# Kernel optimization log

Measured on AMD Instinct MI355X. Metric: run time of the kernel, lower is better.

## Reference

```python
import jax, jax.numpy as jnp
import numpy as np

N_SLOTS, SLOT_DIM, FEAT_DIM, N_HEADS = 8, 256, 128, 4
HEAD_DIM = SLOT_DIM // N_HEADS
B, H, W = 32, 64, 64


def layernorm(x, g, b, eps=1e-5):
    mu = jnp.mean(x, axis=-1, keepdims=True)
    var = jnp.var(x, axis=-1, keepdims=True)
    return (x - mu) * jax.lax.rsqrt(var + eps) * g + b


def setup_inputs() -> dict:
    key = jax.random.key(0)
    ks = jax.random.split(key, 20)
    s = lambda i, shape, sc: (jax.random.normal(ks[i], shape, dtype=jnp.float32) * sc)
    return {
        'features': s(0, (B, FEAT_DIM, H, W), 1.0),
        'slots': s(1, (B, N_SLOTS, SLOT_DIM), 1.0),
        'Wq': s(2, (SLOT_DIM, SLOT_DIM), 0.05), 'bq': jnp.zeros((SLOT_DIM,), jnp.float32),
        'Wk': s(3, (FEAT_DIM, SLOT_DIM), 0.05), 'bk': jnp.zeros((SLOT_DIM,), jnp.float32),
        'Wv': s(4, (FEAT_DIM, SLOT_DIM), 0.05), 'bv': jnp.zeros((SLOT_DIM,), jnp.float32),
        'W_ih': s(5, (3 * SLOT_DIM, SLOT_DIM), 0.05), 'b_ih': jnp.zeros((3 * SLOT_DIM,), jnp.float32),
        'W_hh': s(6, (3 * SLOT_DIM, SLOT_DIM), 0.05), 'b_hh': jnp.zeros((3 * SLOT_DIM,), jnp.float32),
        'g_pre': jnp.ones((SLOT_DIM,), jnp.float32), 'b_pre': jnp.zeros((SLOT_DIM,), jnp.float32),
        'g_post': jnp.ones((SLOT_DIM,), jnp.float32), 'b_post': jnp.zeros((SLOT_DIM,), jnp.float32),
        'W1': s(7, (SLOT_DIM, 2 * SLOT_DIM), 0.05), 'b1': jnp.zeros((2 * SLOT_DIM,), jnp.float32),
        'W2': s(8, (2 * SLOT_DIM, SLOT_DIM), 0.05), 'b2': jnp.zeros((SLOT_DIM,), jnp.float32),
    }


def reference(features, slots, Wq, bq, Wk, bk, Wv, bv, W_ih, b_ih, W_hh, b_hh,
              g_pre, b_pre, g_post, b_post, W1, b1, W2, b2):
    b, c, h, w = features.shape
    n = h * w
    feats = features.transpose(0, 2, 3, 1).reshape(b, n, c)  # (B, HW, C)

    slots_n = layernorm(slots, g_pre, b_pre)
    q = (slots_n @ Wq + bq).reshape(b, N_SLOTS, N_HEADS, HEAD_DIM)
    k = (feats @ Wk + bk).reshape(b, n, N_HEADS, HEAD_DIM)
    v = (feats @ Wv + bv).reshape(b, n, N_HEADS, HEAD_DIM)

    scale = HEAD_DIM ** -0.5
    # scores: (B, heads, slots, HW); softmax over the SLOT axis (competition)
    scores = jnp.einsum('bshd,bnhd->bhsn', q, k) * scale
    attn = jax.nn.softmax(scores, axis=2)
    agg = jnp.einsum('bhsn,bnhd->bshd', attn, v).reshape(b, N_SLOTS, SLOT_DIM)

    # GRUCell (torch semantics): gates ordered r, z, n
    x = agg.reshape(b * N_SLOTS, SLOT_DIM)
    hprev = slots.reshape(b * N_SLOTS, SLOT_DIM)
    gi = x @ W_ih.T + b_ih
    gh = hprev @ W_hh.T + b_hh
    i_r, i_z, i_n = jnp.split(gi, 3, axis=-1)
    h_r, h_z, h_n = jnp.split(gh, 3, axis=-1)
    r = jax.nn.sigmoid(i_r + h_r)
    z = jax.nn.sigmoid(i_z + h_z)
    nn_ = jnp.tanh(i_n + r * h_n)
    hnew = (1.0 - z) * nn_ + z * hprev
    updated = hnew.reshape(b, N_SLOTS, SLOT_DIM)

    # post-norm + MLP residual (dropout is identity in eval)
    refined = jax.nn.relu(layernorm(updated, g_post, b_post) @ W1 + b1) @ W2 + b2
    return updated + refined
```

## Files before the change

kernel.cpp:

```cpp
#include <hip/hip_runtime.h>
#include <hip/hip_bf16.h>

#define NSLOT 8
#define SDIM 256
#define FDIM 128
#define NHEAD 4
#define HDIM 64
#define NPOS 4096

typedef short v8s __attribute__((ext_vector_type(8)));
typedef short v4s __attribute__((ext_vector_type(4)));
typedef float v4f __attribute__((ext_vector_type(4)));

__device__ __forceinline__ unsigned short f2bf(float x) {
    __hip_bfloat16 h = __float2bfloat16(x);
    unsigned short u; __builtin_memcpy(&u, &h, 2); return u;
}
__device__ __forceinline__ float bfr2f(unsigned short u) {
    __hip_bfloat16 h; __builtin_memcpy(&h, &u, 2); return __bfloat162float(h);
}
__device__ __forceinline__ void splitf(float x, unsigned short& hi, unsigned short& lo) {
    hi = f2bf(x);
    lo = f2bf(x - bfr2f(hi));
}

__global__ __launch_bounds__(256) void k_prep(
    const float* __restrict__ slots,
    const float* __restrict__ Wq, const float* __restrict__ bq,
    const float* __restrict__ g_pre, const float* __restrict__ b_pre,
    const float* __restrict__ Wk, const float* __restrict__ bk,
    const float* __restrict__ W1, const float* __restrict__ W2,
    const float* __restrict__ W_ih, const float* __restrict__ W_hh,
    const float* __restrict__ Wv,
    unsigned short* __restrict__ qkT_ws, float* __restrict__ qb_ws,
    unsigned short* __restrict__ W1Th, unsigned short* __restrict__ W1Tl,
    unsigned short* __restrict__ W2Th, unsigned short* __restrict__ W2Tl,
    unsigned short* __restrict__ WihH, unsigned short* __restrict__ WihL,
    unsigned short* __restrict__ WhhH, unsigned short* __restrict__ WhhL,
    unsigned short* __restrict__ WvTH, unsigned short* __restrict__ WvTl,
    float* __restrict__ agg_ws)
{
    int blk = blockIdx.x, t = threadIdx.x;
    __shared__ float s_ln[8 * 256];
    __shared__ float q_l[32 * 65];
    __shared__ float red1[256], red2[256];
    __shared__ float tl[32][33];

    if (blk >= 560) {
        int id3 = blk - 560;
        int k0 = (id3 & 3) * 32, n0 = (id3 >> 2) * 32;
        for (int i = 0; i < 4; i++) {
            int idx = i * 256 + t, r = idx >> 5, c = idx & 31;
            tl[r][c] = Wv[(size_t)(k0 + r) * 256 + n0 + c];
        }
        __syncthreads();
        for (int i = 0; i < 4; i++) {
            int idx = i * 256 + t, r = idx >> 5, c = idx & 31;
            unsigned short hi, lo; splitf(tl[c][r], hi, lo);
            WvTH[(size_t)(n0 + r) * 128 + k0 + c] = hi;
            WvTl[(size_t)(n0 + r) * 128 + k0 + c] = lo;
        }
        return;
    }
    if (blk >= 512) {
        int id2 = blk - 512;
        const float* src; unsigned short *dh, *dl; int r0;
        if (id2 < 24) { src = W_ih; dh = WihH; dl = WihL; r0 = id2 * 32; }
        else          { src = W_hh; dh = WhhH; dl = WhhL; r0 = (id2 - 24) * 32; }
        for (int i = 0; i < 32; i++) {
            size_t idx = (size_t)(r0 + i) * 256 + t;
            unsigned short hi, lo; splitf(src[idx], hi, lo);
            dh[idx] = hi; dl[idx] = lo;
        }
        return;
    }
    if (blk >= 256) {
        int id = blk - 256;
        const float* src; unsigned short *dh, *dl; int N, K, k0, n0;
        if (id < 128) { src = W1; dh = W1Th; dl = W1Tl; N = 512; K = 256;
                        k0 = (id >> 4) * 32; n0 = (id & 15) * 32; }
        else          { int i2 = id - 128; src = W2; dh = W2Th; dl = W2Tl; N = 256; K = 512;
                        k0 = (i2 >> 3) * 32; n0 = (i2 & 7) * 32; }
        for (int i = 0; i < 4; i++) {
            int idx = i * 256 + t, r = idx >> 5, c = idx & 31;
            tl[r][c] = src[(size_t)(k0 + r) * N + n0 + c];
        }
        __syncthreads();
        for (int i = 0; i < 4; i++) {
            int idx = i * 256 + t, r = idx >> 5, c = idx & 31;
            unsigned short hi, lo; splitf(tl[c][r], hi, lo);
            dh[(size_t)(n0 + r) * K + k0 + c] = hi;
            dl[(size_t)(n0 + r) * K + k0 + c] = lo;
        }
        return;
    }

    int b = blk >> 3, chunk = blk & 7;
    if (chunk == 0)
        for (int i = 0; i < 8; i++) agg_ws[b * 2048 + i * 256 + t] = 0.0f;

    int s8 = t >> 5, lane = t & 31;
    float xv[8], sum = 0.0f, sq = 0.0f;
    for (int u = 0; u < 8; u++) {
        float x = slots[(b * 8 + s8) * 256 + lane * 8 + u];
        xv[u] = x; sum += x; sq += x * x;
    }
    red1[t] = sum; red2[t] = sq;
    __syncthreads();
    for (int o = 16; o > 0; o >>= 1) {
        if (lane < o) { red1[t] += red1[t + o]; red2[t] += red2[t + o]; }
        __syncthreads();
    }
    float mu  = red1[s8 * 32] * (1.0f / 256);
    float var = red2[s8 * 32] * (1.0f / 256) - mu * mu;
    float rstd = rsqrtf(var + 1e-5f);
    for (int u = 0; u < 8; u++) {
        int j = lane * 8 + u;
        s_ln[s8 * 256 + j] = (xv[u] - mu) * rstd * g_pre[j] + b_pre[j];
    }
    __syncthreads();

    float qa[8];
    #pragma unroll
    for (int s = 0; s < 8; s++) qa[s] = bq[t];
    for (int k = 0; k < 256; k++) {
        float wq = Wq[k * 256 + t];
        #pragma unroll
        for (int s = 0; s < 8; s++) qa[s] += s_ln[s * 256 + k] * wq;
    }
    int h = t >> 6, d = t & 63;
    for (int s = 0; s < 8; s++) q_l[(s * 4 + h) * 65 + d] = qa[s];
    __syncthreads();

    int hs = t & 31, hh = hs >> 3, si = hs & 7, c0 = t >> 5;
    const float* qrow = &q_l[(si * 4 + hh) * 65];
    for (int i = 0; i < 2; i++) {
        int c = chunk * 16 + i * 8 + c0;
        const float4* wk4 = (const float4*)&Wk[c * 256 + hh * 64];
        float acc = 0.0f;
        #pragma unroll
        for (int d4 = 0; d4 < 16; d4++) {
            float4 w = wk4[d4];
            acc += w.x * qrow[d4 * 4] + w.y * qrow[d4 * 4 + 1]
                 + w.z * qrow[d4 * 4 + 2] + w.w * qrow[d4 * 4 + 3];
        }
        qkT_ws[(b * 32 + hs) * 128 + c] = f2bf(acc);
    }
    if (chunk == 0 && t < 32) {
        int h2 = t >> 3, s2 = t & 7;
        float acc = 0.0f;
        for (int d2 = 0; d2 < 64; d2++)
            acc += bk[h2 * 64 + d2] * q_l[(s2 * 4 + h2) * 65 + d2];
        qb_ws[b * 32 + t] = acc;
    }
}

__global__ __launch_bounds__(256, 4) void k_attn(
    const float* __restrict__ feat,
    const unsigned short* __restrict__ WvTH, const unsigned short* __restrict__ WvTl,
    const float* __restrict__ bv,
    const unsigned short* __restrict__ qkT, const float* __restrict__ qb_ws,
    float* __restrict__ agg_ws)
{
    __shared__ __align__(16) char smem[31360];
    unsigned short* featPC = (unsigned short*)smem;
    unsigned short* featCP = (unsigned short*)(smem + 8704);
    unsigned short* attFH  = (unsigned short*)smem;
    unsigned short* attFL  = (unsigned short*)(smem + 8704);
    float*          s_attn = (float*)(smem + 23040);
    unsigned short* s_aT   = (unsigned short*)(smem + 27648);
    float*          s_S    = (float*)(smem + 31232);

    int t = threadIdx.x, b = blockIdx.y, n0 = blockIdx.x * 128;
    int wv_ = t >> 6, lane = t & 63, quad = lane >> 4, l16 = lane & 15;
    int mt = wv_ >> 1, nt = wv_ & 1;
    int sp  = l16 + mt * 16;
    int shs = l16 + nt * 16;

    v8s bq_[4];
    #pragma unroll
    for (int ch = 0; ch < 4; ch++)
        bq_[ch] = *(const v8s*)&qkT[(b * 32 + shs) * 128 + ch * 32 + quad * 8];
    float qbv = qb_ws[b * 32 + shs];
    if (t < 32) s_S[t] = 0.0f;

    v4f accF[4];
    #pragma unroll
    for (int i = 0; i < 4; i++) accF[i] = (v4f){0.f, 0.f, 0.f, 0.f};

    int c0 = (t >> 3) * 4, p0 = (t & 7) * 4;

    for (int tt = 0; tt < 4; ++tt) {
        __syncthreads();
        int nb = n0 + tt * 32;
        float fv[4][4];
        #pragma unroll
        for (int r = 0; r < 4; r++) {
            float4 f = *(const float4*)&feat[(size_t)b * (FDIM * NPOS)
                                             + (size_t)(c0 + r) * NPOS + nb + p0];
            fv[r][0] = f.x; fv[r][1] = f.y; fv[r][2] = f.z; fv[r][3] = f.w;
        }
        #pragma unroll
        for (int r = 0; r < 4; r++)
            *(v4s*)&featCP[(c0 + r) * 56 + p0] =
                (v4s){(short)f2bf(fv[r][0]), (short)f2bf(fv[r][1]),
                      (short)f2bf(fv[r][2]), (short)f2bf(fv[r][3])};
        #pragma unroll
        for (int j = 0; j < 4; j++)
            *(v4s*)&featPC[(p0 + j) * 136 + c0] =
                (v4s){(short)f2bf(fv[0][j]), (short)f2bf(fv[1][j]),
                      (short)f2bf(fv[2][j]), (short)f2bf(fv[3][j])};
        __syncthreads();

        v4f acc = (v4f){0.f, 0.f, 0.f, 0.f};
        #pragma unroll
        for (int ch = 0; ch < 4; ch++) {
            v8s a = *(const v8s*)&featPC[sp * 136 + ch * 32 + quad * 8];
            acc = __builtin_amdgcn_mfma_f32_16x16x32_bf16(a, bq_[ch], acc, 0, 0, 0);
        }
        int pb = mt * 16 + quad * 4;
        #pragma unroll
        for (int r = 0; r < 4; r++)
            s_attn[(pb + r) * 36 + shs] = (acc[r] + qbv) * 0.125f;
        __syncthreads();

        if (t < 128) {
            int p = t >> 2, h2 = t & 3;
            float* a = &s_attn[p * 36 + h2 * 8];
            float m = a[0];
            for (int s = 1; s < 8; s++) m = fmaxf(m, a[s]);
            float e[8], ssum = 0.0f;
            for (int s = 0; s < 8; s++) { e[s] = __expf(a[s] - m); ssum += e[s]; }
            float inv = 1.0f / ssum;
            for (int s = 0; s < 8; s++)
                s_aT[(h2 * 8 + s) * 56 + p] = f2bf(e[s] * inv);
        }
        __syncthreads();

        v8s aA0 = *(const v8s*)&s_aT[l16 * 56 + quad * 8];
        v8s aA1 = *(const v8s*)&s_aT[(l16 + 16) * 56 + quad * 8];
        v8s bF0 = *(const v8s*)&featCP[(l16 + wv_ * 32) * 56 + quad * 8];
        v8s bF1 = *(const v8s*)&featCP[(l16 + wv_ * 32 + 16) * 56 + quad * 8];
        accF[0] = __builtin_amdgcn_mfma_f32_16x16x32_bf16(aA0, bF0, accF[0], 0, 0, 0);
        accF[1] = __builtin_amdgcn_mfma_f32_16x16x32_bf16(aA0, bF1, accF[1], 0, 0, 0);
        accF[2] = __builtin_amdgcn_mfma_f32_16x16x32_bf16(aA1, bF0, accF[2], 0, 0, 0);
        accF[3] = __builtin_amdgcn_mfma_f32_16x16x32_bf16(aA1, bF1, accF[3], 0, 0, 0);
        if (t < 32) {
            float ss = 0.0f;
            for (int p = 0; p < 32; p++) ss += bfr2f(s_aT[t * 56 + p]);
            s_S[t] += ss;
        }
    }
    __syncthreads();
    #pragma unroll
    for (int mt2 = 0; mt2 < 2; mt2++)
        #pragma unroll
        for (int ntl = 0; ntl < 2; ntl++) {
            v4f f = accF[mt2 * 2 + ntl];
            int cc = wv_ * 32 + ntl * 16 + l16;
            #pragma unroll
            for (int r = 0; r < 4; r++) {
                unsigned short hi, lo; splitf(f[r], hi, lo);
                attFH[(mt2 * 16 + quad * 4 + r) * 136 + cc] = hi;
                attFL[(mt2 * 16 + quad * 4 + r) * 136 + cc] = lo;
            }
        }
    __syncthreads();

    int h = wv_;
    int am = h * 8 + (l16 & 7);
    for (int nt2 = 0; nt2 < 4; nt2++) {
        int n = h * 64 + nt2 * 16 + l16;
        v4f acc = (v4f){0.f, 0.f, 0.f, 0.f};
        #pragma unroll
        for (int kk = 0; kk < 4; kk++) {
            int ko = kk * 32 + quad * 8;
            v8s ah = *(const v8s*)&attFH[am * 136 + ko];
            v8s al = *(const v8s*)&attFL[am * 136 + ko];
            v8s bh = *(const v8s*)&WvTH[(size_t)n * 128 + ko];
            v8s bl = *(const v8s*)&WvTl[(size_t)n * 128 + ko];
            acc = __builtin_amdgcn_mfma_f32_16x16x32_bf16(al, bh, acc, 0, 0, 0);
            acc = __builtin_amdgcn_mfma_f32_16x16x32_bf16(ah, bl, acc, 0, 0, 0);
            acc = __builtin_amdgcn_mfma_f32_16x16x32_bf16(ah, bh, acc, 0, 0, 0);
        }
        float bvn = bv[n];
        if (quad < 2) {
            #pragma unroll
            for (int r = 0; r < 4; r++) {
                int s = quad * 4 + r;
                atomicAdd(&agg_ws[b * 2048 + s * 256 + n],
                          acc[r] + s_S[h * 8 + s] * bvn);
            }
        }
    }
}

__global__ __launch_bounds__(256) void k_gate(
    const float* __restrict__ agg, const float* __restrict__ slots,
    const unsigned short* __restrict__ WihH, const unsigned short* __restrict__ WihL,
    const float* __restrict__ b_ih,
    const unsigned short* __restrict__ WhhH, const unsigned short* __restrict__ WhhL,
    const float* __restrict__ b_hh,
    float* __restrict__ G)
{
    int ntile = blockIdx.x, mtile = blockIdx.y, t = threadIdx.x;
    bool hhalf = ntile >= 12;
    int jbase = (hhalf ? ntile - 12 : ntile) * 64;
    const float* X = hhalf ? slots : agg;
    const unsigned short* BH = hhalf ? WhhH : WihH;
    const unsigned short* BL = hhalf ? WhhL : WihL;
    const float* bias = hhalf ? b_hh : b_ih;
    int gofs = hhalf ? 768 : 0;
    int m0 = mtile * 64;

    __shared__ __align__(16) unsigned short aH[64][264];
    __shared__ __align__(16) unsigned short aL[64][264];
    for (int i = 0; i < 16; i++) {
        int idx = i * 256 + t;
        int r = idx >> 6, q = idx & 63;
        float4 f = *(const float4*)&X[(size_t)(m0 + r) * 256 + q * 4];
        unsigned short h0,l0,h1,l1,h2,l2,h3,l3;
        splitf(f.x, h0, l0); splitf(f.y, h1, l1);
        splitf(f.z, h2, l2); splitf(f.w, h3, l3);
        *(v4s*)&aH[r][q * 4] = (v4s){(short)h0,(short)h1,(short)h2,(short)h3};
        *(v4s*)&aL[r][q * 4] = (v4s){(short)l0,(short)l1,(short)l2,(short)l3};
    }
    __syncthreads();

    int w = t >> 6, lane = t & 63, quad = lane >> 4, l16 = lane & 15;
    int am = w * 16 + l16;
    for (int s = 0; s < 4; s++) {
        int jrow = jbase + s * 16 + l16;
        v4f acc = (v4f){0.f, 0.f, 0.f, 0.f};
        #pragma unroll
        for (int kk = 0; kk < 8; kk++) {
            int ko = kk * 32 + quad * 8;
            v8s ah = *(const v8s*)&aH[am][ko];
            v8s al = *(const v8s*)&aL[am][ko];
            v8s bh = *(const v8s*)&BH[(size_t)jrow * 256 + ko];
            v8s bl = *(const v8s*)&BL[(size_t)jrow * 256 + ko];
            acc = __builtin_amdgcn_mfma_f32_16x16x32_bf16(al, bh, acc, 0, 0, 0);
            acc = __builtin_amdgcn_mfma_f32_16x16x32_bf16(ah, bl, acc, 0, 0, 0);
            acc = __builtin_amdgcn_mfma_f32_16x16x32_bf16(ah, bh, acc, 0, 0, 0);
        }
        float bv_ = bias[jrow];
        int gj = gofs + jbase + s * 16 + l16;
        #pragma unroll
        for (int r = 0; r < 4; r++)
            G[(size_t)(m0 + w * 16 + quad * 4 + r) * 1536 + gj] = acc[r] + bv_;
    }
}

__device__ __forceinline__ float gru1(float ir, float iz, float in_,
                                      float hr, float hz, float hn, float hp) {
    float r = 1.0f / (1.0f + __expf(-(ir + hr)));
    float z = 1.0f / (1.0f + __expf(-(iz + hz)));
    float n = tanhf(in_ + r * hn);
    return (1.0f - z) * n + z * hp;
}

__global__ __launch_bounds__(1024) void k_tail2(
    const float* __restrict__ slots, const float* __restrict__ G,
    const float* __restrict__ g_post, const float* __restrict__ b_post,
    const unsigned short* __restrict__ W1Th, const unsigned short* __restrict__ W1Tl,
    const float* __restrict__ b1,
    const unsigned short* __restrict__ W2Th, const unsigned short* __restrict__ W2Tl,
    const float* __restrict__ b2,
    float* __restrict__ hnF, float* __restrict__ out)
{
    __shared__ __align__(16) char smem[50176];
    unsigned short* lnH   = (unsigned short*)smem;
    unsigned short* lnLo  = (unsigned short*)(smem + 8448);
    unsigned short* y1H   = (unsigned short*)(smem + 16896);
    unsigned short* y1Lo  = (unsigned short*)(smem + 33536);

    int t = threadIdx.x, m0 = blockIdx.x * 16;
    int w = t >> 6, lane = t & 63, quad = lane >> 4, l16 = lane & 15;

    {
        int row = m0 + w, c0 = lane * 4;
        const float* gp = &G[(size_t)row * 1536 + c0];
        float4 gir = *(const float4*)(gp);
        float4 giz = *(const float4*)(gp + 256);
        float4 gin = *(const float4*)(gp + 512);
        float4 ghr = *(const float4*)(gp + 768);
        float4 ghz = *(const float4*)(gp + 1024);
        float4 ghn = *(const float4*)(gp + 1280);
        float4 hp  = *(const float4*)&slots[(size_t)row * 256 + c0];
        float h0 = gru1(gir.x, giz.x, gin.x, ghr.x, ghz.x, ghn.x, hp.x);
        float h1 = gru1(gir.y, giz.y, gin.y, ghr.y, ghz.y, ghn.y, hp.y);
        float h2 = gru1(gir.z, giz.z, gin.z, ghr.z, ghz.z, ghn.z, hp.z);
        float h3 = gru1(gir.w, giz.w, gin.w, ghr.w, ghz.w, ghn.w, hp.w);
        float ssum = h0 + h1 + h2 + h3;
        float ssq  = h0*h0 + h1*h1 + h2*h2 + h3*h3;
        #pragma unroll
        for (int m = 1; m <= 32; m <<= 1) {
            ssum += __shfl_xor(ssum, m, 64);
            ssq  += __shfl_xor(ssq, m, 64);
        }
        float mu = ssum * (1.0f / 256);
        float var = ssq * (1.0f / 256) - mu * mu;
        float rstd = rsqrtf(var + 1e-5f);
        float4 gp4 = *(const float4*)&g_post[c0];
        float4 bp4 = *(const float4*)&b_post[c0];
        float l0 = (h0 - mu) * rstd * gp4.x + bp4.x;
        float l1 = (h1 - mu) * rstd * gp4.y + bp4.y;
        float l2 = (h2 - mu) * rstd * gp4.z + bp4.z;
        float l3 = (h3 - mu) * rstd * gp4.w + bp4.w;
        unsigned short a0,c0s,a1,c1s,a2,c2s,a3,c3s;
        splitf(l0, a0, c0s); splitf(l1, a1, c1s);
        splitf(l2, a2, c2s); splitf(l3, a3, c3s);
        *(v4s*)&lnH[w * 264 + c0]  = (v4s){(short)a0,(short)a1,(short)a2,(short)a3};
        *(v4s*)&lnLo[w * 264 + c0] = (v4s){(short)c0s,(short)c1s,(short)c2s,(short)c3s};
        float4 hv4; hv4.x = h0; hv4.y = h1; hv4.z = h2; hv4.w = h3;
        *(float4*)&hnF[(size_t)row * 256 + c0] = hv4;
    }
    __syncthreads();

    #pragma unroll
    for (int i = 0; i < 2; i++) {
        int ntile = w * 2 + i;
        int n = ntile * 16 + l16;
        v4f acc = (v4f){0.f, 0.f, 0.f, 0.f};
        #pragma unroll
        for (int kk = 0; kk < 8; kk++) {
            int ko = kk * 32 + quad * 8;
            v8s ah = *(const v8s*)&lnH[l16 * 264 + ko];
            v8s al = *(const v8s*)&lnLo[l16 * 264 + ko];
            v8s bh = *(const v8s*)&W1Th[(size_t)n * 256 + ko];
            v8s bl = *(const v8s*)&W1Tl[(size_t)n * 256 + ko];
            acc = __builtin_amdgcn_mfma_f32_16x16x32_bf16(al, bh, acc, 0, 0, 0);
            acc = __builtin_amdgcn_mfma_f32_16x16x32_bf16(ah, bl, acc, 0, 0, 0);
            acc = __builtin_amdgcn_mfma_f32_16x16x32_bf16(ah, bh, acc, 0, 0, 0);
        }
        float bb = b1[n];
        #pragma unroll
        for (int r = 0; r < 4; r++) {
            float y = fmaxf(acc[r] + bb, 0.0f);
            unsigned short hi, lo; splitf(y, hi, lo);
            y1H[(quad * 4 + r) * 520 + n]  = hi;
            y1Lo[(quad * 4 + r) * 520 + n] = lo;
        }
    }
    __syncthreads();

    {
        int n = w * 16 + l16;
        v4f acc = (v4f){0.f, 0.f, 0.f, 0.f};
        #pragma unroll
        for (int kk = 0; kk < 16; kk++) {
            int ko = kk * 32 + quad * 8;
            v8s ah = *(const v8s*)&y1H[l16 * 520 + ko];
            v8s al = *(const v8s*)&y1Lo[l16 * 520 + ko];
            v8s bh = *(const v8s*)&W2Th[(size_t)n * 512 + ko];
            v8s bl = *(const v8s*)&W2Tl[(size_t)n * 512 + ko];
            acc = __builtin_amdgcn_mfma_f32_16x16x32_bf16(al, bh, acc, 0, 0, 0);
            acc = __builtin_amdgcn_mfma_f32_16x16x32_bf16(ah, bl, acc, 0, 0, 0);
            acc = __builtin_amdgcn_mfma_f32_16x16x32_bf16(ah, bh, acc, 0, 0, 0);
        }
        float bb = b2[n];
        #pragma unroll
        for (int r = 0; r < 4; r++) {
            int m = m0 + quad * 4 + r;
            out[(size_t)m * 256 + n] = hnF[(size_t)m * 256 + n] + acc[r] + bb;
        }
    }
}

extern "C" void kernel_launch(void* const* d_in, const int* in_sizes, int n_in,
                              void* d_out, int out_size, void* d_ws, size_t ws_size,
                              hipStream_t stream) {
    const float* features = (const float*)d_in[0];
    const float* slots    = (const float*)d_in[1];
    const float* Wq   = (const float*)d_in[2];
    const float* bq   = (const float*)d_in[3];
    const float* Wk   = (const float*)d_in[4];
    const float* bk   = (const float*)d_in[5];
    const float* Wv   = (const float*)d_in[6];
    const float* bv   = (const float*)d_in[7];
    const float* W_ih = (const float*)d_in[8];
    const float* b_ih = (const float*)d_in[9];
    const float* W_hh = (const float*)d_in[10];
    const float* b_hh = (const float*)d_in[11];
    const float* g_pre  = (const float*)d_in[12];
    const float* b_pre  = (const float*)d_in[13];
    const float* g_post = (const float*)d_in[14];
    const float* b_post = (const float*)d_in[15];
    const float* W1 = (const float*)d_in[16];
    const float* b1 = (const float*)d_in[17];
    const float* W2 = (const float*)d_in[18];
    const float* b2 = (const float*)d_in[19];
    float* out = (float*)d_out;

    char* wsb = (char*)d_ws;
    float* G               = (float*)wsb;
    unsigned short* qkT_ws = (unsigned short*)wsb;
    float* qb_ws           = (float*)(wsb + 262144);
    unsigned short* W1Th   = (unsigned short*)(wsb + 1572864);
    unsigned short* W1Tl   = (unsigned short*)(wsb + 1835008);
    unsigned short* W2Th   = (unsigned short*)(wsb + 2097152);
    unsigned short* W2Tl   = (unsigned short*)(wsb + 2359296);
    unsigned short* WihH   = (unsigned short*)(wsb + 2621440);
    unsigned short* WihL   = (unsigned short*)(wsb + 3014656);
    unsigned short* WhhH   = (unsigned short*)(wsb + 3407872);
    unsigned short* WhhL   = (unsigned short*)(wsb + 3801088);
    unsigned short* WvTH   = (unsigned short*)(wsb + 4194304);
    unsigned short* WvTl   = (unsigned short*)(wsb + 4259840);
    float* hnF             = (float*)(wsb + 4325376);
    float* agg_ws = out;

    k_prep<<<dim3(592), dim3(256), 0, stream>>>(
        slots, Wq, bq, g_pre, b_pre, Wk, bk, W1, W2, W_ih, W_hh, Wv,
        qkT_ws, qb_ws, W1Th, W1Tl, W2Th, W2Tl,
        WihH, WihL, WhhH, WhhL, WvTH, WvTl, agg_ws);
    k_attn<<<dim3(32, 32), dim3(256), 0, stream>>>(
        features, WvTH, WvTl, bv, qkT_ws, qb_ws, agg_ws);
    k_gate<<<dim3(24, 4), dim3(256), 0, stream>>>(
        agg_ws, slots, WihH, WihL, b_ih, WhhH, WhhL, b_hh, G);
    k_tail2<<<dim3(16), dim3(1024), 0, stream>>>(
        slots, G, g_post, b_post, W1Th, W1Tl, b1, W2Th, W2Tl, b2, hnF, out);
}
```

Measured before the change: 210.2 us.

## Fuse GRU gate GEMM into tail kernel, prefetch features, shuffle-reduce attention sums

The separate k_gate kernel and its G workspace round-trip are removed. The gate GEMMs now run inside the 1024-thread tail kernel, with each wave computing all six gate tiles for its 16 columns. LayerNorm statistics are then reduced across waves through shared memory. Separately, k_attn register-prefetches the next feature tile before the MFMA work and computes per-slot attention sums with warp shuffles and atomics instead of a serial 32-thread loop, and the Wq projection in k_prep is unrolled by 4 with float4 shared loads. The fused tail uses only 16 blocks for the gate GEMM, which lowers parallelism compared with the former 96 blocks.

```diff
diff --git a/kernel.cpp b/kernel.cpp
--- a/kernel.cpp
+++ b/kernel.cpp
@@ -41,7 +41,7 @@
     float* __restrict__ agg_ws)
 {
     int blk = blockIdx.x, t = threadIdx.x;
-    __shared__ float s_ln[8 * 256];
+    __shared__ __align__(16) float s_ln[8 * 256];
     __shared__ float q_l[32 * 65];
     __shared__ float red1[256], red2[256];
     __shared__ float tl[32][33];
@@ -123,10 +123,16 @@
     float qa[8];
     #pragma unroll
     for (int s = 0; s < 8; s++) qa[s] = bq[t];
-    for (int k = 0; k < 256; k++) {
-        float wq = Wq[k * 256 + t];
-        #pragma unroll
-        for (int s = 0; s < 8; s++) qa[s] += s_ln[s * 256 + k] * wq;
+    for (int k = 0; k < 256; k += 4) {
+        float w0 = Wq[(k + 0) * 256 + t];
+        float w1 = Wq[(k + 1) * 256 + t];
+        float w2 = Wq[(k + 2) * 256 + t];
+        float w3 = Wq[(k + 3) * 256 + t];
+        #pragma unroll
+        for (int s = 0; s < 8; s++) {
+            float4 sl4 = *(const float4*)&s_ln[s * 256 + k];
+            qa[s] += sl4.x * w0 + sl4.y * w1 + sl4.z * w2 + sl4.w * w3;
+        }
     }
     int h = t >> 6, d = t & 63;
     for (int s = 0; s < 8; s++) q_l[(s * 4 + h) * 65 + d] = qa[s];
@@ -189,28 +195,41 @@
     for (int i = 0; i < 4; i++) accF[i] = (v4f){0.f, 0.f, 0.f, 0.f};
 
     int c0 = (t >> 3) * 4, p0 = (t & 7) * 4;
-
+    size_t fbase = (size_t)b * (FDIM * NPOS);
+
+    float fv[4][4];
+    #pragma unroll
+    for (int r = 0; r < 4; r++) {
+        float4 f = *(const float4*)&feat[fbase + (size_t)(c0 + r) * NPOS + n0 + p0];
+        fv[r][0] = f.x; fv[r][1] = f.y; fv[r][2] = f.z; fv[r][3] = f.w;
+    }
+
+    #pragma unroll
     for (int tt = 0; tt < 4; ++tt) {
         __syncthreads();
-        int nb = n0 + tt * 32;
-        float fv[4][4];
-        #pragma unroll
-        for (int r = 0; r < 4; r++) {
-            float4 f = *(const float4*)&feat[(size_t)b * (FDIM * NPOS)
-                                             + (size_t)(c0 + r) * NPOS + nb + p0];
-            fv[r][0] = f.x; fv[r][1] = f.y; fv[r][2] = f.z; fv[r][3] = f.w;
-        }
+        unsigned short us[4][4];
+        #pragma unroll
+        for (int r = 0; r < 4; r++)
+            #pragma unroll
+            for (int j = 0; j < 4; j++) us[r][j] = f2bf(fv[r][j]);
         #pragma unroll
         for (int r = 0; r < 4; r++)
             *(v4s*)&featCP[(c0 + r) * 56 + p0] =
-                (v4s){(short)f2bf(fv[r][0]), (short)f2bf(fv[r][1]),
-                      (short)f2bf(fv[r][2]), (short)f2bf(fv[r][3])};
+                (v4s){(short)us[r][0], (short)us[r][1], (short)us[r][2], (short)us[r][3]};
         #pragma unroll
         for (int j = 0; j < 4; j++)
             *(v4s*)&featPC[(p0 + j) * 136 + c0] =
-                (v4s){(short)f2bf(fv[0][j]), (short)f2bf(fv[1][j]),
-                      (short)f2bf(fv[2][j]), (short)f2bf(fv[3][j])};
-        __syncthreads();
+                (v4s){(short)us[0][j], (short)us[1][j], (short)us[2][j], (short)us[3][j]};
+        __syncthreads();
+
+        if (tt < 3) {
+            #pragma unroll
+            for (int r = 0; r < 4; r++) {
+                float4 f = *(const float4*)&feat[fbase + (size_t)(c0 + r) * NPOS
+                                                 + n0 + (tt + 1) * 32 + p0];
+                fv[r][0] = f.x; fv[r][1] = f.y; fv[r][2] = f.z; fv[r][3] = f.w;
+            }
+        }
 
         v4f acc = (v4f){0.f, 0.f, 0.f, 0.f};
         #pragma unroll
@@ -232,8 +251,19 @@
             float e[8], ssum = 0.0f;
             for (int s = 0; s < 8; s++) { e[s] = __expf(a[s] - m); ssum += e[s]; }
             float inv = 1.0f / ssum;
-            for (int s = 0; s < 8; s++)
-                s_aT[(h2 * 8 + s) * 56 + p] = f2bf(e[s] * inv);
+            float sv[8];
+            #pragma unroll
+            for (int s = 0; s < 8; s++) {
+                sv[s] = e[s] * inv;
+                s_aT[(h2 * 8 + s) * 56 + p] = f2bf(sv[s]);
+            }
+            #pragma unroll
+            for (int mm = 4; mm <= 32; mm <<= 1)
+                #pragma unroll
+                for (int s = 0; s < 8; s++) sv[s] += __shfl_xor(sv[s], mm, 64);
+            if ((t & 63) < 4)
+                #pragma unroll
+                for (int s = 0; s < 8; s++) atomicAdd(&s_S[h2 * 8 + s], sv[s]);
         }
         __syncthreads();
 
@@ -245,11 +275,6 @@
         accF[1] = __builtin_amdgcn_mfma_f32_16x16x32_bf16(aA0, bF1, accF[1], 0, 0, 0);
         accF[2] = __builtin_amdgcn_mfma_f32_16x16x32_bf16(aA1, bF0, accF[2], 0, 0, 0);
         accF[3] = __builtin_amdgcn_mfma_f32_16x16x32_bf16(aA1, bF1, accF[3], 0, 0, 0);
-        if (t < 32) {
-            float ss = 0.0f;
-            for (int p = 0; p < 32; p++) ss += bfr2f(s_aT[t * 56 + p]);
-            s_S[t] += ss;
-        }
     }
     __syncthreads();
     #pragma unroll
@@ -295,62 +320,6 @@
     }
 }
 
-__global__ __launch_bounds__(256) void k_gate(
-    const float* __restrict__ agg, const float* __restrict__ slots,
-    const unsigned short* __restrict__ WihH, const unsigned short* __restrict__ WihL,
-    const float* __restrict__ b_ih,
-    const unsigned short* __restrict__ WhhH, const unsigned short* __restrict__ WhhL,
-    const float* __restrict__ b_hh,
-    float* __restrict__ G)
-{
-    int ntile = blockIdx.x, mtile = blockIdx.y, t = threadIdx.x;
-    bool hhalf = ntile >= 12;
-    int jbase = (hhalf ? ntile - 12 : ntile) * 64;
-    const float* X = hhalf ? slots : agg;
-    const unsigned short* BH = hhalf ? WhhH : WihH;
-    const unsigned short* BL = hhalf ? WhhL : WihL;
-    const float* bias = hhalf ? b_hh : b_ih;
-    int gofs = hhalf ? 768 : 0;
-    int m0 = mtile * 64;
-
-    __shared__ __align__(16) unsigned short aH[64][264];
-    __shared__ __align__(16) unsigned short aL[64][264];
-    for (int i = 0; i < 16; i++) {
-        int idx = i * 256 + t;
-        int r = idx >> 6, q = idx & 63;
-        float4 f = *(const float4*)&X[(size_t)(m0 + r) * 256 + q * 4];
-        unsigned short h0,l0,h1,l1,h2,l2,h3,l3;
-        splitf(f.x, h0, l0); splitf(f.y, h1, l1);
-        splitf(f.z, h2, l2); splitf(f.w, h3, l3);
-        *(v4s*)&aH[r][q * 4] = (v4s){(short)h0,(short)h1,(short)h2,(short)h3};
-        *(v4s*)&aL[r][q * 4] = (v4s){(short)l0,(short)l1,(short)l2,(short)l3};
-    }
-    __syncthreads();
-
-    int w = t >> 6, lane = t & 63, quad = lane >> 4, l16 = lane & 15;
-    int am = w * 16 + l16;
-    for (int s = 0; s < 4; s++) {
-        int jrow = jbase + s * 16 + l16;
-        v4f acc = (v4f){0.f, 0.f, 0.f, 0.f};
-        #pragma unroll
-        for (int kk = 0; kk < 8; kk++) {
-            int ko = kk * 32 + quad * 8;
-            v8s ah = *(const v8s*)&aH[am][ko];
-            v8s al = *(const v8s*)&aL[am][ko];
-            v8s bh = *(const v8s*)&BH[(size_t)jrow * 256 + ko];
-            v8s bl = *(const v8s*)&BL[(size_t)jrow * 256 + ko];
-            acc = __builtin_amdgcn_mfma_f32_16x16x32_bf16(al, bh, acc, 0, 0, 0);
-            acc = __builtin_amdgcn_mfma_f32_16x16x32_bf16(ah, bl, acc, 0, 0, 0);
-            acc = __builtin_amdgcn_mfma_f32_16x16x32_bf16(ah, bh, acc, 0, 0, 0);
-        }
-        float bv_ = bias[jrow];
-        int gj = gofs + jbase + s * 16 + l16;
-        #pragma unroll
-        for (int r = 0; r < 4; r++)
-            G[(size_t)(m0 + w * 16 + quad * 4 + r) * 1536 + gj] = acc[r] + bv_;
-    }
-}
-
 __device__ __forceinline__ float gru1(float ir, float iz, float in_,
                                       float hr, float hz, float hn, float hp) {
     float r = 1.0f / (1.0f + __expf(-(ir + hr)));
@@ -359,8 +328,12 @@
     return (1.0f - z) * n + z * hp;
 }
 
-__global__ __launch_bounds__(1024) void k_tail2(
-    const float* __restrict__ slots, const float* __restrict__ G,
+__global__ __launch_bounds__(1024) void k_gate_tail(
+    const float* __restrict__ agg, const float* __restrict__ slots,
+    const unsigned short* __restrict__ WihH, const unsigned short* __restrict__ WihL,
+    const float* __restrict__ b_ih,
+    const unsigned short* __restrict__ WhhH, const unsigned short* __restrict__ WhhL,
+    const float* __restrict__ b_hh,
     const float* __restrict__ g_post, const float* __restrict__ b_post,
     const unsigned short* __restrict__ W1Th, const unsigned short* __restrict__ W1Tl,
     const float* __restrict__ b1,
@@ -368,52 +341,127 @@
     const float* __restrict__ b2,
     float* __restrict__ hnF, float* __restrict__ out)
 {
-    __shared__ __align__(16) char smem[50176];
-    unsigned short* lnH   = (unsigned short*)smem;
-    unsigned short* lnLo  = (unsigned short*)(smem + 8448);
-    unsigned short* y1H   = (unsigned short*)(smem + 16896);
-    unsigned short* y1Lo  = (unsigned short*)(smem + 33536);
+    __shared__ __align__(16) char smem[54400];
+    unsigned short* aggH = (unsigned short*)smem;
+    unsigned short* aggL = (unsigned short*)(smem + 8448);
+    unsigned short* slH  = (unsigned short*)(smem + 16896);
+    unsigned short* slL  = (unsigned short*)(smem + 25344);
+    unsigned short* lnH  = (unsigned short*)smem;
+    unsigned short* lnLo = (unsigned short*)(smem + 8448);
+    unsigned short* y1H  = (unsigned short*)(smem + 16896);
+    unsigned short* y1Lo = (unsigned short*)(smem + 33536);
+    float* partS = (float*)(smem + 50176);
+    float* partQ = (float*)(smem + 52224);
+    float* muS   = (float*)(smem + 54272);
+    float* rsS   = (float*)(smem + 54336);
 
     int t = threadIdx.x, m0 = blockIdx.x * 16;
     int w = t >> 6, lane = t & 63, quad = lane >> 4, l16 = lane & 15;
 
     {
-        int row = m0 + w, c0 = lane * 4;
-        const float* gp = &G[(size_t)row * 1536 + c0];
-        float4 gir = *(const float4*)(gp);
-        float4 giz = *(const float4*)(gp + 256);
-        float4 gin = *(const float4*)(gp + 512);
-        float4 ghr = *(const float4*)(gp + 768);
-        float4 ghz = *(const float4*)(gp + 1024);
-        float4 ghn = *(const float4*)(gp + 1280);
-        float4 hp  = *(const float4*)&slots[(size_t)row * 256 + c0];
-        float h0 = gru1(gir.x, giz.x, gin.x, ghr.x, ghz.x, ghn.x, hp.x);
-        float h1 = gru1(gir.y, giz.y, gin.y, ghr.y, ghz.y, ghn.y, hp.y);
-        float h2 = gru1(gir.z, giz.z, gin.z, ghr.z, ghz.z, ghn.z, hp.z);
-        float h3 = gru1(gir.w, giz.w, gin.w, ghr.w, ghz.w, ghn.w, hp.w);
-        float ssum = h0 + h1 + h2 + h3;
-        float ssq  = h0*h0 + h1*h1 + h2*h2 + h3*h3;
-        #pragma unroll
-        for (int m = 1; m <= 32; m <<= 1) {
-            ssum += __shfl_xor(ssum, m, 64);
-            ssq  += __shfl_xor(ssq, m, 64);
-        }
-        float mu = ssum * (1.0f / 256);
-        float var = ssq * (1.0f / 256) - mu * mu;
-        float rstd = rsqrtf(var + 1e-5f);
-        float4 gp4 = *(const float4*)&g_post[c0];
-        float4 bp4 = *(const float4*)&b_post[c0];
-        float l0 = (h0 - mu) * rstd * gp4.x + bp4.x;
-        float l1 = (h1 - mu) * rstd * gp4.y + bp4.y;
-        float l2 = (h2 - mu) * rstd * gp4.z + bp4.z;
-        float l3 = (h3 - mu) * rstd * gp4.w + bp4.w;
-        unsigned short a0,c0s,a1,c1s,a2,c2s,a3,c3s;
-        splitf(l0, a0, c0s); splitf(l1, a1, c1s);
-        splitf(l2, a2, c2s); splitf(l3, a3, c3s);
-        *(v4s*)&lnH[w * 264 + c0]  = (v4s){(short)a0,(short)a1,(short)a2,(short)a3};
-        *(v4s*)&lnLo[w * 264 + c0] = (v4s){(short)c0s,(short)c1s,(short)c2s,(short)c3s};
-        float4 hv4; hv4.x = h0; hv4.y = h1; hv4.z = h2; hv4.w = h3;
-        *(float4*)&hnF[(size_t)row * 256 + c0] = hv4;
+        int r = t >> 6, c4 = (t & 63) * 4;
+        float4 f = *(const float4*)&agg[(size_t)(m0 + r) * 256 + c4];
+        unsigned short h0,l0,h1,l1,h2,l2,h3,l3;
+        splitf(f.x, h0, l0); splitf(f.y, h1, l1);
+        splitf(f.z, h2, l2); splitf(f.w, h3, l3);
+        *(v4s*)&aggH[r * 264 + c4] = (v4s){(short)h0,(short)h1,(short)h2,(short)h3};
+        *(v4s*)&aggL[r * 264 + c4] = (v4s){(short)l0,(short)l1,(short)l2,(short)l3};
+        float4 g = *(const float4*)&slots[(size_t)(m0 + r) * 256 + c4];
+        splitf(g.x, h0, l0); splitf(g.y, h1, l1);
+        splitf(g.z, h2, l2); splitf(g.w, h3, l3);
+        *(v4s*)&slH[r * 264 + c4] = (v4s){(short)h0,(short)h1,(short)h2,(short)h3};
+        *(v4s*)&slL[r * 264 + c4] = (v4s){(short)l0,(short)l1,(short)l2,(short)l3};
+    }
+    __syncthreads();
+
+    int j0 = w * 16, jc = j0 + l16;
+    v4f ir = (v4f){0.f,0.f,0.f,0.f}, iz = ir, inn = ir;
+    v4f hrA = ir, hzA = ir, hnA = ir;
+    #pragma unroll
+    for (int kk = 0; kk < 8; kk++) {
+        int ko = kk * 32 + quad * 8;
+        v8s xah = *(const v8s*)&aggH[l16 * 264 + ko];
+        v8s xal = *(const v8s*)&aggL[l16 * 264 + ko];
+        v8s hah = *(const v8s*)&slH[l16 * 264 + ko];
+        v8s hal = *(const v8s*)&slL[l16 * 264 + ko];
+        size_t r0w = (size_t)jc * 256 + ko;
+        size_t r1w = (size_t)(256 + jc) * 256 + ko;
+        size_t r2w = (size_t)(512 + jc) * 256 + ko;
+        v8s bh, bl;
+        bh = *(const v8s*)&WihH[r0w]; bl = *(const v8s*)&WihL[r0w];
+        ir  = __builtin_amdgcn_mfma_f32_16x16x32_bf16(xal, bh, ir,  0, 0, 0);
+        ir  = __builtin_amdgcn_mfma_f32_16x16x32_bf16(xah, bl, ir,  0, 0, 0);
+        ir  = __builtin_amdgcn_mfma_f32_16x16x32_bf16(xah, bh, ir,  0, 0, 0);
+        bh = *(const v8s*)&WihH[r1w]; bl = *(const v8s*)&WihL[r1w];
+        iz  = __builtin_amdgcn_mfma_f32_16x16x32_bf16(xal, bh, iz,  0, 0, 0);
+        iz  = __builtin_amdgcn_mfma_f32_16x16x32_bf16(xah, bl, iz,  0, 0, 0);
+        iz  = __builtin_amdgcn_mfma_f32_16x16x32_bf16(xah, bh, iz,  0, 0, 0);
+        bh = *(const v8s*)&WihH[r2w]; bl = *(const v8s*)&WihL[r2w];
+        inn = __builtin_amdgcn_mfma_f32_16x16x32_bf16(xal, bh, inn, 0, 0, 0);
+        inn = __builtin_amdgcn_mfma_f32_16x16x32_bf16(xah, bl, inn, 0, 0, 0);
+        inn = __builtin_amdgcn_mfma_f32_16x16x32_bf16(xah, bh, inn, 0, 0, 0);
+        bh = *(const v8s*)&WhhH[r0w]; bl = *(const v8s*)&WhhL[r0w];
+        hrA = __builtin_amdgcn_mfma_f32_16x16x32_bf16(hal, bh, hrA, 0, 0, 0);
+        hrA = __builtin_amdgcn_mfma_f32_16x16x32_bf16(hah, bl, hrA, 0, 0, 0);
+        hrA = __builtin_amdgcn_mfma_f32_16x16x32_bf16(hah, bh, hrA, 0, 0, 0);
+        bh = *(const v8s*)&WhhH[r1w]; bl = *(const v8s*)&WhhL[r1w];
+        hzA = __builtin_amdgcn_mfma_f32_16x16x32_bf16(hal, bh, hzA, 0, 0, 0);
+        hzA = __builtin_amdgcn_mfma_f32_16x16x32_bf16(hah, bl, hzA, 0, 0, 0);
+        hzA = __builtin_amdgcn_mfma_f32_16x16x32_bf16(hah, bh, hzA, 0, 0, 0);
+        bh = *(const v8s*)&WhhH[r2w]; bl = *(const v8s*)&WhhL[r2w];
+        hnA = __builtin_amdgcn_mfma_f32_16x16x32_bf16(hal, bh, hnA, 0, 0, 0);
+        hnA = __builtin_amdgcn_mfma_f32_16x16x32_bf16(hah, bl, hnA, 0, 0, 0);
+        hnA = __builtin_amdgcn_mfma_f32_16x16x32_bf16(hah, bh, hnA, 0, 0, 0);
+    }
+
+    float bir = b_ih[jc], biz = b_ih[256 + jc], bin_ = b_ih[512 + jc];
+    float bhr = b_hh[jc], bhz = b_hh[256 + jc], bhn = b_hh[512 + jc];
+    float hnew[4];
+    #pragma unroll
+    for (int r = 0; r < 4; r++) {
+        int m = m0 + quad * 4 + r;
+        float hp = slots[(size_t)m * 256 + jc];
+        hnew[r] = gru1(ir[r] + bir, iz[r] + biz, inn[r] + bin_,
+                       hrA[r] + bhr, hzA[r] + bhz, hnA[r] + bhn, hp);
+        hnF[(size_t)m * 256 + jc] = hnew[r];
+    }
+    float ps[4], pq[4];
+    #pragma unroll
+    for (int r = 0; r < 4; r++) { ps[r] = hnew[r]; pq[r] = hnew[r] * hnew[r]; }
+    #pragma unroll
+    for (int mm = 1; mm <= 8; mm <<= 1)
+        #pragma unroll
+        for (int r = 0; r < 4; r++) {
+            ps[r] += __shfl_xor(ps[r], mm, 64);
+            pq[r] += __shfl_xor(pq[r], mm, 64);
+        }
+    if (l16 == 0)
+        #pragma unroll
+        for (int r = 0; r < 4; r++) {
+            partS[w * 16 + quad * 4 + r] = ps[r];
+            partQ[w * 16 + quad * 4 + r] = pq[r];
+        }
+    __syncthreads();
+    if (t < 16) {
+        float s = 0.0f, q = 0.0f;
+        for (int ww = 0; ww < 16; ww++) {
+            s += partS[ww * 16 + t]; q += partQ[ww * 16 + t];
+        }
+        float mu = s * (1.0f / 256);
+        float var = q * (1.0f / 256) - mu * mu;
+        muS[t] = mu; rsS[t] = rsqrtf(var + 1e-5f);
+    }
+    __syncthreads();
+    {
+        float gp = g_post[jc], bp = b_post[jc];
+        #pragma unroll
+        for (int r = 0; r < 4; r++) {
+            int row = quad * 4 + r;
+            float ln = (hnew[r] - muS[row]) * rsS[row] * gp + bp;
+            unsigned short hi, lo; splitf(ln, hi, lo);
+            lnH[row * 264 + jc]  = hi;
+            lnLo[row * 264 + jc] = lo;
+        }
     }
     __syncthreads();
 
@@ -493,7 +541,6 @@
     float* out = (float*)d_out;
 
     char* wsb = (char*)d_ws;
-    float* G               = (float*)wsb;
     unsigned short* qkT_ws = (unsigned short*)wsb;
     float* qb_ws           = (float*)(wsb + 262144);
     unsigned short* W1Th   = (unsigned short*)(wsb + 1572864);
@@ -515,8 +562,7 @@
         WihH, WihL, WhhH, WhhL, WvTH, WvTl, agg_ws);
     k_attn<<<dim3(32, 32), dim3(256), 0, stream>>>(
         features, WvTH, WvTl, bv, qkT_ws, qb_ws, agg_ws);
-    k_gate<<<dim3(24, 4), dim3(256), 0, stream>>>(
-        agg_ws, slots, WihH, WihL, b_ih, WhhH, WhhL, b_hh, G);
-    k_tail2<<<dim3(16), dim3(1024), 0, stream>>>(
-        slots, G, g_post, b_post, W1Th, W1Tl, b1, W2Th, W2Tl, b2, hnF, out);
-}
+    k_gate_tail<<<dim3(16), dim3(1024), 0, stream>>>(
+        agg_ws, slots, WihH, WihL, b_ih, WhhH, WhhL, b_hh,
+        g_post, b_post, W1Th, W1Tl, b1, W2Th, W2Tl, b2, hnF, out);
+}
```

Result: slower. 232.8 us (+10.8%).

## Restructure prep, prefetch features in attention, warp-reduce slot sums, retile gate GEMM

Applied to the files above, without the earlier changes.

k_prep now uses one block per batch, which computes all 128 qk columns, so the redundant per-chunk LayerNorm and Wq projection is gone and the grid shrinks. The Wq loop is unrolled by four with float4 shared loads. k_attn prefetches the next feature tile into registers before the compute of the current tile, and replaces the serial 32-thread column sum of attention weights with wavefront shuffles plus shared atomics. k_gate uses 16-row tiles, giving four times as many blocks to raise parallelism, at the cost of reloading B weights more often.

```diff
diff --git a/kernel.cpp b/kernel.cpp
--- a/kernel.cpp
+++ b/kernel.cpp
@@ -41,13 +41,13 @@
     float* __restrict__ agg_ws)
 {
     int blk = blockIdx.x, t = threadIdx.x;
-    __shared__ float s_ln[8 * 256];
+    __shared__ __align__(16) float s_ln[8 * 256];
     __shared__ float q_l[32 * 65];
     __shared__ float red1[256], red2[256];
     __shared__ float tl[32][33];
 
-    if (blk >= 560) {
-        int id3 = blk - 560;
+    if (blk >= 336) {
+        int id3 = blk - 336;
         int k0 = (id3 & 3) * 32, n0 = (id3 >> 2) * 32;
         for (int i = 0; i < 4; i++) {
             int idx = i * 256 + t, r = idx >> 5, c = idx & 31;
@@ -62,8 +62,8 @@
         }
         return;
     }
-    if (blk >= 512) {
-        int id2 = blk - 512;
+    if (blk >= 288) {
+        int id2 = blk - 288;
         const float* src; unsigned short *dh, *dl; int r0;
         if (id2 < 24) { src = W_ih; dh = WihH; dl = WihL; r0 = id2 * 32; }
         else          { src = W_hh; dh = WhhH; dl = WhhL; r0 = (id2 - 24) * 32; }
@@ -74,8 +74,8 @@
         }
         return;
     }
-    if (blk >= 256) {
-        int id = blk - 256;
+    if (blk >= 32) {
+        int id = blk - 32;
         const float* src; unsigned short *dh, *dl; int N, K, k0, n0;
         if (id < 128) { src = W1; dh = W1Th; dl = W1Tl; N = 512; K = 256;
                         k0 = (id >> 4) * 32; n0 = (id & 15) * 32; }
@@ -95,9 +95,8 @@
         return;
     }
 
-    int b = blk >> 3, chunk = blk & 7;
-    if (chunk == 0)
-        for (int i = 0; i < 8; i++) agg_ws[b * 2048 + i * 256 + t] = 0.0f;
+    int b = blk;
+    for (int i = 0; i < 8; i++) agg_ws[b * 2048 + i * 256 + t] = 0.0f;
 
     int s8 = t >> 5, lane = t & 31;
     float xv[8], sum = 0.0f, sq = 0.0f;
@@ -123,10 +122,16 @@
     float qa[8];
     #pragma unroll
     for (int s = 0; s < 8; s++) qa[s] = bq[t];
-    for (int k = 0; k < 256; k++) {
-        float wq = Wq[k * 256 + t];
-        #pragma unroll
-        for (int s = 0; s < 8; s++) qa[s] += s_ln[s * 256 + k] * wq;
+    for (int k = 0; k < 256; k += 4) {
+        float w0 = Wq[(k + 0) * 256 + t];
+        float w1 = Wq[(k + 1) * 256 + t];
+        float w2 = Wq[(k + 2) * 256 + t];
+        float w3 = Wq[(k + 3) * 256 + t];
+        #pragma unroll
+        for (int s = 0; s < 8; s++) {
+            float4 sl4 = *(const float4*)&s_ln[s * 256 + k];
+            qa[s] += sl4.x * w0 + sl4.y * w1 + sl4.z * w2 + sl4.w * w3;
+        }
     }
     int h = t >> 6, d = t & 63;
     for (int s = 0; s < 8; s++) q_l[(s * 4 + h) * 65 + d] = qa[s];
@@ -134,8 +139,8 @@
 
     int hs = t & 31, hh = hs >> 3, si = hs & 7, c0 = t >> 5;
     const float* qrow = &q_l[(si * 4 + hh) * 65];
-    for (int i = 0; i < 2; i++) {
-        int c = chunk * 16 + i * 8 + c0;
+    for (int i = 0; i < 16; i++) {
+        int c = i * 8 + c0;
         const float4* wk4 = (const float4*)&Wk[c * 256 + hh * 64];
         float acc = 0.0f;
         #pragma unroll
@@ -146,7 +151,7 @@
         }
         qkT_ws[(b * 32 + hs) * 128 + c] = f2bf(acc);
     }
-    if (chunk == 0 && t < 32) {
+    if (t < 32) {
         int h2 = t >> 3, s2 = t & 7;
         float acc = 0.0f;
         for (int d2 = 0; d2 < 64; d2++)
@@ -189,28 +194,41 @@
     for (int i = 0; i < 4; i++) accF[i] = (v4f){0.f, 0.f, 0.f, 0.f};
 
     int c0 = (t >> 3) * 4, p0 = (t & 7) * 4;
-
+    size_t fbase = (size_t)b * (FDIM * NPOS);
+
+    float fv[4][4];
+    #pragma unroll
+    for (int r = 0; r < 4; r++) {
+        float4 f = *(const float4*)&feat[fbase + (size_t)(c0 + r) * NPOS + n0 + p0];
+        fv[r][0] = f.x; fv[r][1] = f.y; fv[r][2] = f.z; fv[r][3] = f.w;
+    }
+
+    #pragma unroll
     for (int tt = 0; tt < 4; ++tt) {
         __syncthreads();
-        int nb = n0 + tt * 32;
-        float fv[4][4];
-        #pragma unroll
-        for (int r = 0; r < 4; r++) {
-            float4 f = *(const float4*)&feat[(size_t)b * (FDIM * NPOS)
-                                             + (size_t)(c0 + r) * NPOS + nb + p0];
-            fv[r][0] = f.x; fv[r][1] = f.y; fv[r][2] = f.z; fv[r][3] = f.w;
-        }
+        unsigned short us[4][4];
+        #pragma unroll
+        for (int r = 0; r < 4; r++)
+            #pragma unroll
+            for (int j = 0; j < 4; j++) us[r][j] = f2bf(fv[r][j]);
         #pragma unroll
         for (int r = 0; r < 4; r++)
             *(v4s*)&featCP[(c0 + r) * 56 + p0] =
-                (v4s){(short)f2bf(fv[r][0]), (short)f2bf(fv[r][1]),
-                      (short)f2bf(fv[r][2]), (short)f2bf(fv[r][3])};
+                (v4s){(short)us[r][0], (short)us[r][1], (short)us[r][2], (short)us[r][3]};
         #pragma unroll
         for (int j = 0; j < 4; j++)
             *(v4s*)&featPC[(p0 + j) * 136 + c0] =
-                (v4s){(short)f2bf(fv[0][j]), (short)f2bf(fv[1][j]),
-                      (short)f2bf(fv[2][j]), (short)f2bf(fv[3][j])};
-        __syncthreads();
+                (v4s){(short)us[0][j], (short)us[1][j], (short)us[2][j], (short)us[3][j]};
+        __syncthreads();
+
+        if (tt < 3) {
+            #pragma unroll
+            for (int r = 0; r < 4; r++) {
+                float4 f = *(const float4*)&feat[fbase + (size_t)(c0 + r) * NPOS
+                                                 + n0 + (tt + 1) * 32 + p0];
+                fv[r][0] = f.x; fv[r][1] = f.y; fv[r][2] = f.z; fv[r][3] = f.w;
+            }
+        }
 
         v4f acc = (v4f){0.f, 0.f, 0.f, 0.f};
         #pragma unroll
@@ -232,8 +250,19 @@
             float e[8], ssum = 0.0f;
             for (int s = 0; s < 8; s++) { e[s] = __expf(a[s] - m); ssum += e[s]; }
             float inv = 1.0f / ssum;
-            for (int s = 0; s < 8; s++)
-                s_aT[(h2 * 8 + s) * 56 + p] = f2bf(e[s] * inv);
+            float sv[8];
+            #pragma unroll
+            for (int s = 0; s < 8; s++) {
+                sv[s] = e[s] * inv;
+                s_aT[(h2 * 8 + s) * 56 + p] = f2bf(sv[s]);
+            }
+            #pragma unroll
+            for (int mm = 4; mm <= 32; mm <<= 1)
+                #pragma unroll
+                for (int s = 0; s < 8; s++) sv[s] += __shfl_xor(sv[s], mm, 64);
+            if ((t & 63) < 4)
+                #pragma unroll
+                for (int s = 0; s < 8; s++) atomicAdd(&s_S[h2 * 8 + s], sv[s]);
         }
         __syncthreads();
 
@@ -245,11 +274,6 @@
         accF[1] = __builtin_amdgcn_mfma_f32_16x16x32_bf16(aA0, bF1, accF[1], 0, 0, 0);
         accF[2] = __builtin_amdgcn_mfma_f32_16x16x32_bf16(aA1, bF0, accF[2], 0, 0, 0);
         accF[3] = __builtin_amdgcn_mfma_f32_16x16x32_bf16(aA1, bF1, accF[3], 0, 0, 0);
-        if (t < 32) {
-            float ss = 0.0f;
-            for (int p = 0; p < 32; p++) ss += bfr2f(s_aT[t * 56 + p]);
-            s_S[t] += ss;
-        }
     }
     __syncthreads();
     #pragma unroll
@@ -311,11 +335,11 @@
     const unsigned short* BL = hhalf ? WhhL : WihL;
     const float* bias = hhalf ? b_hh : b_ih;
     int gofs = hhalf ? 768 : 0;
-    int m0 = mtile * 64;
-
-    __shared__ __align__(16) unsigned short aH[64][264];
-    __shared__ __align__(16) unsigned short aL[64][264];
-    for (int i = 0; i < 16; i++) {
+    int m0 = mtile * 16;
+
+    __shared__ __align__(16) unsigned short aH[16][264];
+    __shared__ __align__(16) unsigned short aL[16][264];
+    for (int i = 0; i < 4; i++) {
         int idx = i * 256 + t;
         int r = idx >> 6, q = idx & 63;
         float4 f = *(const float4*)&X[(size_t)(m0 + r) * 256 + q * 4];
@@ -328,27 +352,24 @@
     __syncthreads();
 
     int w = t >> 6, lane = t & 63, quad = lane >> 4, l16 = lane & 15;
-    int am = w * 16 + l16;
-    for (int s = 0; s < 4; s++) {
-        int jrow = jbase + s * 16 + l16;
-        v4f acc = (v4f){0.f, 0.f, 0.f, 0.f};
-        #pragma unroll
-        for (int kk = 0; kk < 8; kk++) {
-            int ko = kk * 32 + quad * 8;
-            v8s ah = *(const v8s*)&aH[am][ko];
-            v8s al = *(const v8s*)&aL[am][ko];
-            v8s bh = *(const v8s*)&BH[(size_t)jrow * 256 + ko];
-            v8s bl = *(const v8s*)&BL[(size_t)jrow * 256 + ko];
-            acc = __builtin_amdgcn_mfma_f32_16x16x32_bf16(al, bh, acc, 0, 0, 0);
-            acc = __builtin_amdgcn_mfma_f32_16x16x32_bf16(ah, bl, acc, 0, 0, 0);
-            acc = __builtin_amdgcn_mfma_f32_16x16x32_bf16(ah, bh, acc, 0, 0, 0);
-        }
-        float bv_ = bias[jrow];
-        int gj = gofs + jbase + s * 16 + l16;
-        #pragma unroll
-        for (int r = 0; r < 4; r++)
-            G[(size_t)(m0 + w * 16 + quad * 4 + r) * 1536 + gj] = acc[r] + bv_;
-    }
+    int jrow = jbase + w * 16 + l16;
+    v4f acc = (v4f){0.f, 0.f, 0.f, 0.f};
+    #pragma unroll
+    for (int kk = 0; kk < 8; kk++) {
+        int ko = kk * 32 + quad * 8;
+        v8s ah = *(const v8s*)&aH[l16][ko];
+        v8s al = *(const v8s*)&aL[l16][ko];
+        v8s bh = *(const v8s*)&BH[(size_t)jrow * 256 + ko];
+        v8s bl = *(const v8s*)&BL[(size_t)jrow * 256 + ko];
+        acc = __builtin_amdgcn_mfma_f32_16x16x32_bf16(al, bh, acc, 0, 0, 0);
+        acc = __builtin_amdgcn_mfma_f32_16x16x32_bf16(ah, bl, acc, 0, 0, 0);
+        acc = __builtin_amdgcn_mfma_f32_16x16x32_bf16(ah, bh, acc, 0, 0, 0);
+    }
+    float bv_ = bias[jrow];
+    int gj = gofs + jbase + w * 16 + l16;
+    #pragma unroll
+    for (int r = 0; r < 4; r++)
+        G[(size_t)(m0 + quad * 4 + r) * 1536 + gj] = acc[r] + bv_;
 }
 
 __device__ __forceinline__ float gru1(float ir, float iz, float in_,
@@ -509,13 +530,13 @@
     float* hnF             = (float*)(wsb + 4325376);
     float* agg_ws = out;
 
-    k_prep<<<dim3(592), dim3(256), 0, stream>>>(
+    k_prep<<<dim3(368), dim3(256), 0, stream>>>(
         slots, Wq, bq, g_pre, b_pre, Wk, bk, W1, W2, W_ih, W_hh, Wv,
         qkT_ws, qb_ws, W1Th, W1Tl, W2Th, W2Tl,
         WihH, WihL, WhhH, WhhL, WvTH, WvTl, agg_ws);
     k_attn<<<dim3(32, 32), dim3(256), 0, stream>>>(
         features, WvTH, WvTl, bv, qkT_ws, qb_ws, agg_ws);
-    k_gate<<<dim3(24, 4), dim3(256), 0, stream>>>(
+    k_gate<<<dim3(24, 16), dim3(256), 0, stream>>>(
         agg_ws, slots, WihH, WihL, b_ih, WhhH, WhhL, b_hh, G);
     k_tail2<<<dim3(16), dim3(1024), 0, stream>>>(
         slots, G, g_post, b_post, W1Th, W1Tl, b1, W2Th, W2Tl, b2, hnF, out);
```

Measured after the change: 213.4 us. Within noise of the previous version (+1.5%).
